# Optimization experiments

Hardware: AMD Instinct MI355X
Metric: run time of the kernel (lower is better)

## Reference

```python
import jax, jax.numpy as jnp
import numpy as np

N = 20000   # nodes
E = 320000  # edges (avg degree 16)
K = 3       # Chebyshev order


def _glorot(key, shape):
    fan_in, fan_out = shape[-2], shape[-1]
    lim = (6.0 / (fan_in + fan_out)) ** 0.5
    return jax.random.uniform(key, shape, minval=-lim, maxval=lim, dtype=jnp.float32)


def setup_inputs() -> dict:
    key = jax.random.key(0)
    ks = jax.random.split(key, 8)
    v = jax.random.normal(ks[0], (N, 86), dtype=jnp.float32)
    edges = jax.random.randint(ks[1], (2, E), 0, N, dtype=jnp.int32)
    W1 = _glorot(ks[2], (K, 86, 128));  b1 = jnp.zeros((128,), jnp.float32)
    W2 = _glorot(ks[3], (K, 128, 256)); b2 = jnp.zeros((256,), jnp.float32)
    W3 = _glorot(ks[4], (K, 256, 512)); b3 = jnp.zeros((512,), jnp.float32)
    return {"v": v, "edges": edges, "W1": W1, "b1": b1,
            "W2": W2, "b2": b2, "W3": W3, "b3": b3}


def _cheb_norm(edges, n):
    # PyG ChebConv with sym norm, lambda_max=2: L_hat = L - I = -D^-1/2 A D^-1/2
    # (diagonal entries from get_laplacian (+1) and add_self_loops (-1) cancel).
    # Self loops are removed before computing the Laplacian -> mask them out.
    row, col = edges[0], edges[1]
    w = (row != col).astype(jnp.float32)
    deg = jax.ops.segment_sum(w, row, num_segments=n)
    dinv = jnp.where(deg > 0, jax.lax.rsqrt(jnp.maximum(deg, 1e-12)), 0.0)
    norm_w = -dinv[row] * w * dinv[col]  # [E]
    return row, col, norm_w


def _cheb_conv(x, row, col, norm_w, W, b):
    # W: [K, in, out]
    def prop(z):  # L_hat @ z via edge gather + segment scatter-add
        return jax.ops.segment_sum(norm_w[:, None] * z[col], row, num_segments=x.shape[0])
    Tx0 = x
    out = Tx0 @ W[0]
    Tx1 = prop(Tx0)
    out = out + Tx1 @ W[1]
    Tx2 = 2.0 * prop(Tx1) - Tx0
    out = out + Tx2 @ W[2]
    return out + b


def reference(v, edges, W1, b1, W2, b2, W3, b3):
    row, col, norm_w = _cheb_norm(edges, v.shape[0])
    nk = jax.random.key(42)
    x1 = jax.nn.relu(_cheb_conv(v, row, col, norm_w, W1, b1))
    x1 = x1 * jax.random.normal(jax.random.fold_in(nk, 1), x1.shape, x1.dtype)
    x2 = jax.nn.relu(_cheb_conv(x1, row, col, norm_w, W2, b2))
    x2 = x2 * jax.random.normal(jax.random.fold_in(nk, 2), x2.shape, x2.dtype)
    x3 = jax.nn.relu(_cheb_conv(x2, row, col, norm_w, W3, b3))
    x3 = x3 * jax.random.normal(jax.random.fold_in(nk, 3), x3.shape, x3.dtype)
    return (x1, x2, x3)
```

## Files before the change

### kernel.cpp

```cpp
#include <hip/hip_runtime.h>
#include <stdint.h>
#include <math.h>

#define DEV static __device__ __forceinline__

typedef __attribute__((ext_vector_type(8))) short bf16x8;
typedef __attribute__((ext_vector_type(4))) float f32x4;
typedef __attribute__((ext_vector_type(8))) unsigned short u16x8;

DEV uint32_t rotl32(uint32_t v, int d) { return (v << d) | (v >> (32 - d)); }

DEV void threefry2x32(uint32_t k0, uint32_t k1, uint32_t& x0, uint32_t& x1) {
  const uint32_t k2 = k0 ^ k1 ^ 0x1BD11BDAu;
  x0 += k0; x1 += k1;
#define TFR(R) { x0 += x1; x1 = rotl32(x1, R) ^ x0; }
  TFR(13) TFR(15) TFR(26) TFR(6)
  x0 += k1; x1 += k2 + 1u;
  TFR(17) TFR(29) TFR(16) TFR(24)
  x0 += k2; x1 += k0 + 2u;
  TFR(13) TFR(15) TFR(26) TFR(6)
  x0 += k0; x1 += k1 + 3u;
  TFR(17) TFR(29) TFR(16) TFR(24)
  x0 += k1; x1 += k2 + 4u;
  TFR(13) TFR(15) TFR(26) TFR(6)
  x0 += k2; x1 += k0 + 5u;
#undef TFR
}

DEV float erfinv_f32(float x) {
  float w = -log1pf(-x * x);
  float p;
  if (w < 5.0f) {
    w -= 2.5f;
    p = 2.81022636e-08f;
    p = fmaf(p, w, 3.43273939e-07f);
    p = fmaf(p, w, -3.5233877e-06f);
    p = fmaf(p, w, -4.39150654e-06f);
    p = fmaf(p, w, 0.00021858087f);
    p = fmaf(p, w, -0.00125372503f);
    p = fmaf(p, w, -0.00417768164f);
    p = fmaf(p, w, 0.246640727f);
    p = fmaf(p, w, 1.50140941f);
  } else {
    w = sqrtf(w) - 3.0f;
    p = -0.000200214257f;
    p = fmaf(p, w, 0.000100950558f);
    p = fmaf(p, w, 0.00134934322f);
    p = fmaf(p, w, -0.00367342844f);
    p = fmaf(p, w, 0.00573950773f);
    p = fmaf(p, w, -0.0076224613f);
    p = fmaf(p, w, 0.00943887047f);
    p = fmaf(p, w, 1.00167406f);
    p = fmaf(p, w, 2.83297682f);
  }
  return p * x;
}

DEV float normal_from_bits(uint32_t bits) {
  float f = __uint_as_float((bits >> 9) | 0x3F800000u) - 1.0f;
  const float lo = -0.99999994f;
  float u = fmaf(f, 2.0f, lo);
  u = fmaxf(u, lo);
  return 1.41421356f * erfinv_f32(u);
}

DEV unsigned short f2bf(float f) {
  uint32_t u = __float_as_uint(f);
  uint32_t r = u + 0x7FFFu + ((u >> 16) & 1u);
  return (unsigned short)(r >> 16);
}

DEV float bf2f(uint32_t h) { return __uint_as_float(h << 16); }

DEV float4 noise4(uint32_t f0, uint32_t f1, uint32_t i4) {
  uint32_t base = i4 * 4u;
  float4 r;
  { uint32_t a = 0u, b = base + 0u; threefry2x32(f0, f1, a, b); r.x = normal_from_bits(a ^ b); }
  { uint32_t a = 0u, b = base + 1u; threefry2x32(f0, f1, a, b); r.y = normal_from_bits(a ^ b); }
  { uint32_t a = 0u, b = base + 2u; threefry2x32(f0, f1, a, b); r.z = normal_from_bits(a ^ b); }
  { uint32_t a = 0u, b = base + 3u; threefry2x32(f0, f1, a, b); r.w = normal_from_bits(a ^ b); }
  return r;
}

__global__ void count_kernel(const int* __restrict__ rows, const int* __restrict__ cols,
                             int* __restrict__ counts, int* __restrict__ degs, int E) {
  int e = blockIdx.x * blockDim.x + threadIdx.x;
  if (e < E) {
    int r = rows[e];
    atomicAdd(&counts[r], 1);
    if (r != cols[e]) atomicAdd(&degs[r], 1);
  }
}

#define SCAN_T 1024
__global__ __launch_bounds__(SCAN_T) void scan_kernel(const int* __restrict__ counts,
                                                      int* __restrict__ row_ptr,
                                                      int* __restrict__ cursor, int N) {
  __shared__ int sa[SCAN_T], sb[SCAN_T];
  const int t = threadIdx.x;
  const int CH = (N + SCAN_T - 1) / SCAN_T;
  int base = t * CH;
  int psum = 0;
  for (int k = 0; k < CH; ++k) {
    int idx = base + k;
    if (idx < N) psum += counts[idx];
  }
  sa[t] = psum;
  __syncthreads();
  int* src = sa; int* dst = sb;
  for (int off = 1; off < SCAN_T; off <<= 1) {
    int v = src[t];
    if (t >= off) v += src[t - off];
    dst[t] = v;
    __syncthreads();
    int* tmp = src; src = dst; dst = tmp;
  }
  int running = src[t] - psum;
  for (int k = 0; k < CH; ++k) {
    int idx = base + k;
    if (idx < N) {
      row_ptr[idx] = running;
      cursor[idx] = running;
      running += counts[idx];
    }
  }
  if (t == SCAN_T - 1) row_ptr[N] = running;
}

__global__ void fill_kernel(const int* __restrict__ rows, const int* __restrict__ cols,
                            const int* __restrict__ degs, int* __restrict__ cursor,
                            float2* __restrict__ ecv, int E) {
  int e = blockIdx.x * blockDim.x + threadIdx.x;
  if (e < E) {
    int r = rows[e], c = cols[e];
    int dr = degs[r], dc = degs[c];
    float w = (r != c && dr > 0 && dc > 0) ? -rsqrtf((float)dr) * rsqrtf((float)dc) : 0.0f;
    int pos = atomicAdd(&cursor[r], 1);
    ecv[pos] = make_float2(__int_as_float(c), w);
  }
}

__global__ void prep_kernel(const float* __restrict__ v,
                            const float* __restrict__ W1, const float* __restrict__ W2,
                            const float* __restrict__ W3,
                            unsigned short* __restrict__ vb, unsigned short* __restrict__ wt1,
                            unsigned short* __restrict__ wt2, unsigned short* __restrict__ wt3,
                            int N) {
  int i = blockIdx.x * 256 + threadIdx.x;
  int nv = N * 96;
  if (i < nv) {
    int r = i / 96, k = i % 96;
    vb[i] = (k < 86) ? f2bf(v[(size_t)r * 86 + k]) : (unsigned short)0;
    return;
  }
  i -= nv;
  if (i < 3 * 128 * 96) {
    int k = i % 96, o = (i / 96) % 128, p = i / (96 * 128);
    wt1[i] = (k < 86) ? f2bf(W1[((size_t)p * 86 + k) * 128 + o]) : (unsigned short)0;
    return;
  }
  i -= 3 * 128 * 96;
  if (i < 3 * 256 * 128) {
    int k = i % 128, o = (i / 128) % 256, p = i / (128 * 256);
    wt2[i] = f2bf(W2[((size_t)p * 128 + k) * 256 + o]);
    return;
  }
  i -= 3 * 256 * 128;
  if (i < 3 * 512 * 256) {
    int k = i % 256, o = (i / 256) % 512, p = i / (256 * 512);
    wt3[i] = f2bf(W3[((size_t)p * 256 + k) * 512 + o]);
  }
}

DEV void ld8(const unsigned short* __restrict__ base, size_t off, float* v) {
  uint4 u = *(const uint4*)(base + off);
  v[0] = bf2f(u.x & 0xffffu); v[1] = bf2f(u.x >> 16);
  v[2] = bf2f(u.y & 0xffffu); v[3] = bf2f(u.y >> 16);
  v[4] = bf2f(u.z & 0xffffu); v[5] = bf2f(u.z >> 16);
  v[6] = bf2f(u.w & 0xffffu); v[7] = bf2f(u.w >> 16);
}

template <int LPN, int NL, int SUB, int FOLD>
__global__ __launch_bounds__(256) void gather_prop(
    const int* __restrict__ row_ptr, const float2* __restrict__ ecv,
    const unsigned short* __restrict__ xsrc, int sstride,
    const float* __restrict__ xsub, int substride, int F,
    unsigned short* __restrict__ outb, int N, int Fpad,
    unsigned short* __restrict__ nbuf, int n4_begin, int n4_end) {
  const int wave = threadIdx.x >> 6, lane = threadIdx.x & 63;
  const int sub = lane / LPN;
  const int fl = (lane - sub * LPN) * 8;
  const int node = (blockIdx.x * 4 + wave) * NL + sub;
  if (sub < NL && node < N) {
    float acc[8] = {};
    const int s = row_ptr[node], e = row_ptr[node + 1];
    int j = s;
    for (; j + 8 <= e; j += 8) {
      float2 cw[8];
      float vv[8][8];
#pragma unroll
      for (int q = 0; q < 8; ++q) cw[q] = ecv[j + q];
#pragma unroll
      for (int q = 0; q < 8; ++q)
        ld8(xsrc, (size_t)__float_as_int(cw[q].x) * sstride + fl, vv[q]);
#pragma unroll
      for (int q = 0; q < 8; ++q)
#pragma unroll
        for (int z = 0; z < 8; ++z) acc[z] = fmaf(cw[q].y, vv[q][z], acc[z]);
    }
    for (; j + 2 <= e; j += 2) {
      float2 cw[2];
      float vv[2][8];
#pragma unroll
      for (int q = 0; q < 2; ++q) cw[q] = ecv[j + q];
#pragma unroll
      for (int q = 0; q < 2; ++q)
        ld8(xsrc, (size_t)__float_as_int(cw[q].x) * sstride + fl, vv[q]);
#pragma unroll
      for (int q = 0; q < 2; ++q)
#pragma unroll
        for (int z = 0; z < 8; ++z) acc[z] = fmaf(cw[q].y, vv[q][z], acc[z]);
    }
    for (; j < e; ++j) {
      float2 cw = ecv[j];
      float vv[8];
      ld8(xsrc, (size_t)__float_as_int(cw.x) * sstride + fl, vv);
#pragma unroll
      for (int z = 0; z < 8; ++z) acc[z] = fmaf(cw.y, vv[z], acc[z]);
    }
    if (SUB) {
      const float* sb = xsub + (size_t)node * substride;
      if (fl + 8 <= F) {
        float4 a = *(const float4*)(sb + fl);
        float4 b2 = *(const float4*)(sb + fl + 4);
        acc[0] = fmaf(2.0f, acc[0], -a.x);  acc[1] = fmaf(2.0f, acc[1], -a.y);
        acc[2] = fmaf(2.0f, acc[2], -a.z);  acc[3] = fmaf(2.0f, acc[3], -a.w);
        acc[4] = fmaf(2.0f, acc[4], -b2.x); acc[5] = fmaf(2.0f, acc[5], -b2.y);
        acc[6] = fmaf(2.0f, acc[6], -b2.z); acc[7] = fmaf(2.0f, acc[7], -b2.w);
      } else {
#pragma unroll
        for (int z = 0; z < 8; ++z) {
          int f = fl + z;
          float sv = (f < F) ? sb[f] : 0.0f;
          acc[z] = fmaf(2.0f, acc[z], -sv);
        }
      }
    }
    uint4 u;
    u.x = (uint32_t)f2bf(acc[0]) | ((uint32_t)f2bf(acc[1]) << 16);
    u.y = (uint32_t)f2bf(acc[2]) | ((uint32_t)f2bf(acc[3]) << 16);
    u.z = (uint32_t)f2bf(acc[4]) | ((uint32_t)f2bf(acc[5]) << 16);
    u.w = (uint32_t)f2bf(acc[6]) | ((uint32_t)f2bf(acc[7]) << 16);
    *(uint4*)&outb[(size_t)node * Fpad + fl] = u;
  }
  uint32_t f0k = 0u, f1k = (uint32_t)FOLD;
  threefry2x32(0u, 42u, f0k, f1k);
  const int gstride = gridDim.x * 256;
  for (int i4 = n4_begin + blockIdx.x * 256 + (int)threadIdx.x; i4 < n4_end; i4 += gstride) {
    float4 r = noise4(f0k, f1k, (uint32_t)i4);
    uint2 u;
    u.x = (uint32_t)f2bf(r.x) | ((uint32_t)f2bf(r.y) << 16);
    u.y = (uint32_t)f2bf(r.z) | ((uint32_t)f2bf(r.w) << 16);
    *(uint2*)&nbuf[(size_t)i4 * 4] = u;
  }
}

template <int BM, int FPAD, int KS, int OB>
__global__ __launch_bounds__(512, 4) void gemm3_db(
    const unsigned short* __restrict__ A0, const unsigned short* __restrict__ A1,
    const unsigned short* __restrict__ A2,
    const unsigned short* __restrict__ Wt, const float* __restrict__ bias,
    const unsigned short* __restrict__ noise,
    int M, int MT, int O, float* __restrict__ out, unsigned short* __restrict__ outb,
    int obstride) {
  constexpr int BN = 128;
  constexpr int NSP = FPAD / KS;
  constexpr int NSTEP = 3 * NSP;
  constexpr int CPR = KS / 8;
  constexpr int LST = KS + 8;
  constexpr int NA = BM * CPR;
  constexpr int NB = BN * CPR;
  constexpr int ACH = (NA + 511) / 512;
  constexpr int BCH = (NB + 511) / 512;
  constexpr int MFR = BM / 32;
  constexpr int KK = KS / 32;

  const int flat = blockIdx.x;
  const int xcd = flat & 7, idx = flat >> 3;
  const int mtile = xcd + 8 * (idx / OB);
  const int obl = idx - (idx / OB) * OB;
  if (mtile >= MT) return;
  const int bm = mtile * BM;
  const int bo = obl * BN;

  __shared__ unsigned short sA[2][BM * LST];
  __shared__ unsigned short sB[2][BN * LST];

  const int tid = threadIdx.x;
  const int lane = tid & 63;
  const int wave = tid >> 6;
  const int wm = wave >> 2, wo = wave & 3;
  const int l15 = lane & 15;
  const int kg = (lane >> 4) * 8;

  f32x4 acc[MFR][2] = {};
  const unsigned short* As[3] = {A0, A1, A2};

  u16x8 ra0[ACH], rb0[BCH], ra1[ACH], rb1[BCH];

  auto issue = [&](int s, u16x8 (&ra)[ACH], u16x8 (&rb)[BCH]) {
    int p = s / NSP, k0 = (s % NSP) * KS;
    const unsigned short* __restrict__ A = As[p];
    const unsigned short* __restrict__ B = Wt + (size_t)p * O * FPAD;
#pragma unroll
    for (int c = 0; c < ACH; ++c) {
      int idx2 = tid + c * 512;
      if (NA % 512 == 0 || idx2 < NA) {
        int row = idx2 / CPR, ch = (idx2 % CPR) * 8;
        int gm = bm + row; if (gm >= M) gm = M - 1;
        ra[c] = *(const u16x8*)(A + (size_t)gm * FPAD + k0 + ch);
      }
    }
#pragma unroll
    for (int c = 0; c < BCH; ++c) {
      int idx2 = tid + c * 512;
      if (NB % 512 == 0 || idx2 < NB) {
        int row = idx2 / CPR, ch = (idx2 % CPR) * 8;
        rb[c] = *(const u16x8*)(B + (size_t)(bo + row) * FPAD + k0 + ch);
      }
    }
  };

  auto lds_write = [&](int buf, u16x8 (&ra)[ACH], u16x8 (&rb)[BCH]) {
#pragma unroll
    for (int c = 0; c < ACH; ++c) {
      int idx2 = tid + c * 512;
      if (NA % 512 == 0 || idx2 < NA) {
        int row = idx2 / CPR, ch = (idx2 % CPR) * 8;
        *(u16x8*)&sA[buf][row * LST + ch] = ra[c];
      }
    }
#pragma unroll
    for (int c = 0; c < BCH; ++c) {
      int idx2 = tid + c * 512;
      if (NB % 512 == 0 || idx2 < NB) {
        int row = idx2 / CPR, ch = (idx2 % CPR) * 8;
        *(u16x8*)&sB[buf][row * LST + ch] = rb[c];
      }
    }
  };

  auto compute = [&](int buf) {
#pragma unroll
    for (int kk = 0; kk < KK; ++kk) {
      bf16x8 af[MFR], bfr[2];
#pragma unroll
      for (int mi = 0; mi < MFR; ++mi)
        af[mi] = *(const bf16x8*)&sA[buf][(wm * (BM / 2) + mi * 16 + l15) * LST + kk * 32 + kg];
#pragma unroll
      for (int ni = 0; ni < 2; ++ni)
        bfr[ni] = *(const bf16x8*)&sB[buf][(wo * 32 + ni * 16 + l15) * LST + kk * 32 + kg];
#pragma unroll
      for (int mi = 0; mi < MFR; ++mi)
#pragma unroll
        for (int ni = 0; ni < 2; ++ni)
          acc[mi][ni] = __builtin_amdgcn_mfma_f32_16x16x32_bf16(af[mi], bfr[ni], acc[mi][ni], 0, 0, 0);
    }
  };

  issue(0, ra0, rb0);
  issue(1, ra1, rb1);
  lds_write(0, ra0, rb0);
  __syncthreads();

#pragma unroll
  for (int s = 0; s < NSTEP; ++s) {
    if ((s & 1) == 0) {
      if (s + 2 < NSTEP) issue(s + 2, ra0, rb0);
      compute(s & 1);
      if (s + 1 < NSTEP) { lds_write((s + 1) & 1, ra1, rb1); __syncthreads(); }
    } else {
      if (s + 2 < NSTEP) issue(s + 2, ra1, rb1);
      compute(s & 1);
      if (s + 1 < NSTEP) { lds_write((s + 1) & 1, ra0, rb0); __syncthreads(); }
    }
  }

  const int r0 = (lane >> 4) * 4;
#pragma unroll
  for (int mi = 0; mi < MFR; ++mi) {
#pragma unroll
    for (int r = 0; r < 4; ++r) {
      int gm = bm + wm * (BM / 2) + mi * 16 + r0 + r;
      if (gm >= M) continue;
#pragma unroll
      for (int ni = 0; ni < 2; ++ni) {
        int go = bo + wo * 32 + ni * 16 + l15;
        float vv = acc[mi][ni][r] + bias[go];
        vv = vv > 0.0f ? vv : 0.0f;
        float res = vv * bf2f((uint32_t)noise[(size_t)gm * O + go]);
        out[(size_t)gm * O + go] = res;
        if (outb) outb[(size_t)gm * obstride + go] = f2bf(res);
      }
    }
  }
}

extern "C" void kernel_launch(void* const* d_in, const int* in_sizes, int n_in,
                              void* d_out, int out_size, void* d_ws, size_t ws_size,
                              hipStream_t stream) {
  const float* v    = (const float*)d_in[0];
  const int*  edges = (const int*)d_in[1];
  const float* W1 = (const float*)d_in[2];
  const float* b1 = (const float*)d_in[3];
  const float* W2 = (const float*)d_in[4];
  const float* b2 = (const float*)d_in[5];
  const float* W3 = (const float*)d_in[6];
  const float* b3 = (const float*)d_in[7];
  float* out = (float*)d_out;

  const int N = in_sizes[0] / 86;
  const int E = in_sizes[1] / 2;
  const int* rows = edges;
  const int* cols = edges + E;

  uintptr_t cur = (uintptr_t)d_ws;
  auto alloc = [&](size_t bytes) {
    cur = (cur + 15) & ~(uintptr_t)15;
    void* p = (void*)cur;
    cur += bytes;
    return p;
  };
  float2* ecv          = (float2*)alloc((size_t)E * 8);
  int* counts          = (int*)alloc((size_t)N * 4);
  int* degs            = (int*)alloc((size_t)N * 4);
  int* row_ptr         = (int*)alloc((size_t)(N + 1) * 4);
  int* cursor          = (int*)alloc((size_t)N * 4);
  unsigned short* tx1b = (unsigned short*)alloc((size_t)N * 256 * 2);
  unsigned short* tx2b = (unsigned short*)alloc((size_t)N * 256 * 2);
  unsigned short* vb   = (unsigned short*)alloc((size_t)N * 96 * 2);
  unsigned short* x1b  = (unsigned short*)alloc((size_t)N * 128 * 2);
  unsigned short* x2b  = (unsigned short*)alloc((size_t)N * 256 * 2);
  unsigned short* wt1  = (unsigned short*)alloc((size_t)3 * 128 * 96 * 2);
  unsigned short* wt2  = (unsigned short*)alloc((size_t)3 * 256 * 128 * 2);
  unsigned short* wt3  = (unsigned short*)alloc((size_t)3 * 512 * 256 * 2);
  unsigned short* nbuf = (unsigned short*)alloc((size_t)N * 512 * 2);

  float* x1 = out;
  float* x2 = x1 + (size_t)N * 128;
  float* x3 = x2 + (size_t)N * 256;

  hipMemsetAsync(counts, 0, (size_t)2 * N * sizeof(int), stream);
  count_kernel<<<(E + 255) / 256, 256, 0, stream>>>(rows, cols, counts, degs, E);
  scan_kernel<<<1, SCAN_T, 0, stream>>>(counts, row_ptr, cursor, N);
  fill_kernel<<<(E + 255) / 256, 256, 0, stream>>>(rows, cols, degs, cursor, ecv, E);
  {
    int total = N * 96 + 3 * 128 * 96 + 3 * 256 * 128 + 3 * 512 * 256;
    prep_kernel<<<(total + 255) / 256, 256, 0, stream>>>(v, W1, W2, W3, vb, wt1, wt2, wt3, N);
  }

  {
    int pb = (N + 15) / 16;
    int t4 = N * 128 / 4, h4 = t4 / 2;
    gather_prop<12, 4, 0, 1><<<pb, 256, 0, stream>>>(row_ptr, ecv, vb, 96, nullptr, 0, 86, tx1b, N, 96, nbuf, 0, h4);
    gather_prop<12, 4, 1, 1><<<pb, 256, 0, stream>>>(row_ptr, ecv, tx1b, 96, v, 86, 86, tx2b, N, 96, nbuf, h4, t4);
    int mt = (N + 63) / 64;
    int grid = 8 * ((mt + 7) / 8) * 1;
    gemm3_db<64, 96, 32, 1><<<grid, 512, 0, stream>>>(vb, tx1b, tx2b, wt1, b1, nbuf, N, mt, 128, x1, x1b, 128);
  }
  {
    int pb = (N + 15) / 16;
    int t4 = N * 256 / 4, h4 = t4 / 2;
    gather_prop<16, 4, 0, 2><<<pb, 256, 0, stream>>>(row_ptr, ecv, x1b, 128, nullptr, 0, 128, tx1b, N, 128, nbuf, 0, h4);
    gather_prop<16, 4, 1, 2><<<pb, 256, 0, stream>>>(row_ptr, ecv, tx1b, 128, x1, 128, 128, tx2b, N, 128, nbuf, h4, t4);
    int mt = (N + 127) / 128;
    int grid = 8 * ((mt + 7) / 8) * 2;
    gemm3_db<128, 128, 64, 2><<<grid, 512, 0, stream>>>(x1b, tx1b, tx2b, wt2, b2, nbuf, N, mt, 256, x2, x2b, 256);
  }
  {
    int pb = (N + 7) / 8;
    int t4 = N * 512 / 4, h4 = t4 / 2;
    gather_prop<32, 2, 0, 3><<<pb, 256, 0, stream>>>(row_ptr, ecv, x2b, 256, nullptr, 0, 256, tx1b, N, 256, nbuf, 0, h4);
    gather_prop<32, 2, 1, 3><<<pb, 256, 0, stream>>>(row_ptr, ecv, tx1b, 256, x2, 256, 256, tx2b, N, 256, nbuf, h4, t4);
    int mt = (N + 127) / 128;
    int grid = 8 * ((mt + 7) / 8) * 4;
    gemm3_db<128, 256, 64, 4><<<grid, 512, 0, stream>>>(x2b, tx1b, tx2b, wt3, b3, nbuf, N, mt, 512, x3, nullptr, 0);
  }
}
```

Baseline: 360.7 us.

## Fold Chebyshev T2 recurrence into weights and move noise generation into GEMM tails

Rewrites the Chebyshev combination algebraically: W0' = W0 - W2 and W2' = 2*W2 are precomputed in prep, so the second propagation becomes a plain L_hat application with no fp32 x read and subtract. This removes the SUB path and its extra fp32 loads from gather_prop. Noise generation also moves out of the gather kernels. Layer-1 noise is now produced in prep_kernel, and the next layer's noise is generated at the end of each GEMM kernel into separate buffers (nb1 aliases nb3). Precision changes slightly, since W0-W2 is rounded to bf16 together and Tx2 is no longer formed explicitly.

Result: slower. 416.4 us (+15.4%).

```diff
diff --git a/kernel.cpp b/kernel.cpp
--- a/kernel.cpp
+++ b/kernel.cpp
@@ -82,6 +82,19 @@
   return r;
 }
 
+DEV void noise_fill(unsigned short* __restrict__ nb, int total4, int fold,
+                    int gbase, int gstride) {
+  uint32_t f0k = 0u, f1k = (uint32_t)fold;
+  threefry2x32(0u, 42u, f0k, f1k);
+  for (int i4 = gbase; i4 < total4; i4 += gstride) {
+    float4 r = noise4(f0k, f1k, (uint32_t)i4);
+    uint2 u;
+    u.x = (uint32_t)f2bf(r.x) | ((uint32_t)f2bf(r.y) << 16);
+    u.y = (uint32_t)f2bf(r.z) | ((uint32_t)f2bf(r.w) << 16);
+    *(uint2*)&nb[(size_t)i4 * 4] = u;
+  }
+}
+
 __global__ void count_kernel(const int* __restrict__ rows, const int* __restrict__ cols,
                              int* __restrict__ counts, int* __restrict__ degs, int E) {
   int e = blockIdx.x * blockDim.x + threadIdx.x;
@@ -145,7 +158,9 @@
                             const float* __restrict__ W3,
                             unsigned short* __restrict__ vb, unsigned short* __restrict__ wt1,
                             unsigned short* __restrict__ wt2, unsigned short* __restrict__ wt3,
-                            int N) {
+                            unsigned short* __restrict__ nb1, int n1_total4, int N) {
+  noise_fill(nb1, n1_total4, 1, blockIdx.x * 256 + threadIdx.x, gridDim.x * 256);
+
   int i = blockIdx.x * 256 + threadIdx.x;
   int nv = N * 96;
   if (i < nv) {
@@ -156,19 +171,33 @@
   i -= nv;
   if (i < 3 * 128 * 96) {
     int k = i % 96, o = (i / 96) % 128, p = i / (96 * 128);
-    wt1[i] = (k < 86) ? f2bf(W1[((size_t)p * 86 + k) * 128 + o]) : (unsigned short)0;
+    float val = 0.0f;
+    if (k < 86) {
+      if (p == 0)      val = W1[((size_t)0 * 86 + k) * 128 + o] - W1[((size_t)2 * 86 + k) * 128 + o];
+      else if (p == 1) val = W1[((size_t)1 * 86 + k) * 128 + o];
+      else             val = 2.0f * W1[((size_t)2 * 86 + k) * 128 + o];
+    }
+    wt1[i] = (k < 86) ? f2bf(val) : (unsigned short)0;
     return;
   }
   i -= 3 * 128 * 96;
   if (i < 3 * 256 * 128) {
     int k = i % 128, o = (i / 128) % 256, p = i / (128 * 256);
-    wt2[i] = f2bf(W2[((size_t)p * 128 + k) * 256 + o]);
+    float val;
+    if (p == 0)      val = W2[((size_t)0 * 128 + k) * 256 + o] - W2[((size_t)2 * 128 + k) * 256 + o];
+    else if (p == 1) val = W2[((size_t)1 * 128 + k) * 256 + o];
+    else             val = 2.0f * W2[((size_t)2 * 128 + k) * 256 + o];
+    wt2[i] = f2bf(val);
     return;
   }
   i -= 3 * 256 * 128;
   if (i < 3 * 512 * 256) {
     int k = i % 256, o = (i / 256) % 512, p = i / (256 * 512);
-    wt3[i] = f2bf(W3[((size_t)p * 256 + k) * 512 + o]);
+    float val;
+    if (p == 0)      val = W3[((size_t)0 * 256 + k) * 512 + o] - W3[((size_t)2 * 256 + k) * 512 + o];
+    else if (p == 1) val = W3[((size_t)1 * 256 + k) * 512 + o];
+    else             val = 2.0f * W3[((size_t)2 * 256 + k) * 512 + o];
+    wt3[i] = f2bf(val);
   }
 }
 
@@ -180,89 +209,58 @@
   v[6] = bf2f(u.w & 0xffffu); v[7] = bf2f(u.w >> 16);
 }
 
-template <int LPN, int NL, int SUB, int FOLD>
+template <int LPN, int NL>
 __global__ __launch_bounds__(256) void gather_prop(
     const int* __restrict__ row_ptr, const float2* __restrict__ ecv,
     const unsigned short* __restrict__ xsrc, int sstride,
-    const float* __restrict__ xsub, int substride, int F,
-    unsigned short* __restrict__ outb, int N, int Fpad,
-    unsigned short* __restrict__ nbuf, int n4_begin, int n4_end) {
+    unsigned short* __restrict__ outb, int N, int Fpad) {
   const int wave = threadIdx.x >> 6, lane = threadIdx.x & 63;
   const int sub = lane / LPN;
   const int fl = (lane - sub * LPN) * 8;
   const int node = (blockIdx.x * 4 + wave) * NL + sub;
-  if (sub < NL && node < N) {
-    float acc[8] = {};
-    const int s = row_ptr[node], e = row_ptr[node + 1];
-    int j = s;
-    for (; j + 8 <= e; j += 8) {
-      float2 cw[8];
-      float vv[8][8];
-#pragma unroll
-      for (int q = 0; q < 8; ++q) cw[q] = ecv[j + q];
-#pragma unroll
-      for (int q = 0; q < 8; ++q)
-        ld8(xsrc, (size_t)__float_as_int(cw[q].x) * sstride + fl, vv[q]);
-#pragma unroll
-      for (int q = 0; q < 8; ++q)
-#pragma unroll
-        for (int z = 0; z < 8; ++z) acc[z] = fmaf(cw[q].y, vv[q][z], acc[z]);
-    }
-    for (; j + 2 <= e; j += 2) {
-      float2 cw[2];
-      float vv[2][8];
-#pragma unroll
-      for (int q = 0; q < 2; ++q) cw[q] = ecv[j + q];
-#pragma unroll
-      for (int q = 0; q < 2; ++q)
-        ld8(xsrc, (size_t)__float_as_int(cw[q].x) * sstride + fl, vv[q]);
-#pragma unroll
-      for (int q = 0; q < 2; ++q)
-#pragma unroll
-        for (int z = 0; z < 8; ++z) acc[z] = fmaf(cw[q].y, vv[q][z], acc[z]);
-    }
-    for (; j < e; ++j) {
-      float2 cw = ecv[j];
-      float vv[8];
-      ld8(xsrc, (size_t)__float_as_int(cw.x) * sstride + fl, vv);
-#pragma unroll
-      for (int z = 0; z < 8; ++z) acc[z] = fmaf(cw.y, vv[z], acc[z]);
-    }
-    if (SUB) {
-      const float* sb = xsub + (size_t)node * substride;
-      if (fl + 8 <= F) {
-        float4 a = *(const float4*)(sb + fl);
-        float4 b2 = *(const float4*)(sb + fl + 4);
-        acc[0] = fmaf(2.0f, acc[0], -a.x);  acc[1] = fmaf(2.0f, acc[1], -a.y);
-        acc[2] = fmaf(2.0f, acc[2], -a.z);  acc[3] = fmaf(2.0f, acc[3], -a.w);
-        acc[4] = fmaf(2.0f, acc[4], -b2.x); acc[5] = fmaf(2.0f, acc[5], -b2.y);
-        acc[6] = fmaf(2.0f, acc[6], -b2.z); acc[7] = fmaf(2.0f, acc[7], -b2.w);
-      } else {
-#pragma unroll
-        for (int z = 0; z < 8; ++z) {
-          int f = fl + z;
-          float sv = (f < F) ? sb[f] : 0.0f;
-          acc[z] = fmaf(2.0f, acc[z], -sv);
-        }
-      }
-    }
-    uint4 u;
-    u.x = (uint32_t)f2bf(acc[0]) | ((uint32_t)f2bf(acc[1]) << 16);
-    u.y = (uint32_t)f2bf(acc[2]) | ((uint32_t)f2bf(acc[3]) << 16);
-    u.z = (uint32_t)f2bf(acc[4]) | ((uint32_t)f2bf(acc[5]) << 16);
-    u.w = (uint32_t)f2bf(acc[6]) | ((uint32_t)f2bf(acc[7]) << 16);
-    *(uint4*)&outb[(size_t)node * Fpad + fl] = u;
-  }
-  uint32_t f0k = 0u, f1k = (uint32_t)FOLD;
-  threefry2x32(0u, 42u, f0k, f1k);
-  const int gstride = gridDim.x * 256;
-  for (int i4 = n4_begin + blockIdx.x * 256 + (int)threadIdx.x; i4 < n4_end; i4 += gstride) {
-    float4 r = noise4(f0k, f1k, (uint32_t)i4);
-    uint2 u;
-    u.x = (uint32_t)f2bf(r.x) | ((uint32_t)f2bf(r.y) << 16);
-    u.y = (uint32_t)f2bf(r.z) | ((uint32_t)f2bf(r.w) << 16);
-    *(uint2*)&nbuf[(size_t)i4 * 4] = u;
-  }
+  if (sub >= NL || node >= N) return;
+  float acc[8] = {};
+  const int s = row_ptr[node], e = row_ptr[node + 1];
+  int j = s;
+  for (; j + 8 <= e; j += 8) {
+    float2 cw[8];
+    float vv[8][8];
+#pragma unroll
+    for (int q = 0; q < 8; ++q) cw[q] = ecv[j + q];
+#pragma unroll
+    for (int q = 0; q < 8; ++q)
+      ld8(xsrc, (size_t)__float_as_int(cw[q].x) * sstride + fl, vv[q]);
+#pragma unroll
+    for (int q = 0; q < 8; ++q)
+#pragma unroll
+      for (int z = 0; z < 8; ++z) acc[z] = fmaf(cw[q].y, vv[q][z], acc[z]);
+  }
+  for (; j + 2 <= e; j += 2) {
+    float2 cw[2];
+    float vv[2][8];
+#pragma unroll
+    for (int q = 0; q < 2; ++q) cw[q] = ecv[j + q];
+#pragma unroll
+    for (int q = 0; q < 2; ++q)
+      ld8(xsrc, (size_t)__float_as_int(cw[q].x) * sstride + fl, vv[q]);
+#pragma unroll
+    for (int q = 0; q < 2; ++q)
+#pragma unroll
+      for (int z = 0; z < 8; ++z) acc[z] = fmaf(cw[q].y, vv[q][z], acc[z]);
+  }
+  for (; j < e; ++j) {
+    float2 cw = ecv[j];
+    float vv[8];
+    ld8(xsrc, (size_t)__float_as_int(cw.x) * sstride + fl, vv);
+#pragma unroll
+    for (int z = 0; z < 8; ++z) acc[z] = fmaf(cw.y, vv[z], acc[z]);
+  }
+  uint4 u;
+  u.x = (uint32_t)f2bf(acc[0]) | ((uint32_t)f2bf(acc[1]) << 16);
+  u.y = (uint32_t)f2bf(acc[2]) | ((uint32_t)f2bf(acc[3]) << 16);
+  u.z = (uint32_t)f2bf(acc[4]) | ((uint32_t)f2bf(acc[5]) << 16);
+  u.w = (uint32_t)f2bf(acc[6]) | ((uint32_t)f2bf(acc[7]) << 16);
+  *(uint4*)&outb[(size_t)node * Fpad + fl] = u;
 }
 
 template <int BM, int FPAD, int KS, int OB>
@@ -272,7 +270,7 @@
     const unsigned short* __restrict__ Wt, const float* __restrict__ bias,
     const unsigned short* __restrict__ noise,
     int M, int MT, int O, float* __restrict__ out, unsigned short* __restrict__ outb,
-    int obstride) {
+    int obstride, unsigned short* __restrict__ nnext, int ntotal4, int nfold) {
   constexpr int BN = 128;
   constexpr int NSP = FPAD / KS;
   constexpr int NSTEP = 3 * NSP;
@@ -289,121 +287,126 @@
   const int xcd = flat & 7, idx = flat >> 3;
   const int mtile = xcd + 8 * (idx / OB);
   const int obl = idx - (idx / OB) * OB;
-  if (mtile >= MT) return;
-  const int bm = mtile * BM;
-  const int bo = obl * BN;
 
   __shared__ unsigned short sA[2][BM * LST];
   __shared__ unsigned short sB[2][BN * LST];
 
   const int tid = threadIdx.x;
-  const int lane = tid & 63;
-  const int wave = tid >> 6;
-  const int wm = wave >> 2, wo = wave & 3;
-  const int l15 = lane & 15;
-  const int kg = (lane >> 4) * 8;
-
-  f32x4 acc[MFR][2] = {};
-  const unsigned short* As[3] = {A0, A1, A2};
-
-  u16x8 ra0[ACH], rb0[BCH], ra1[ACH], rb1[BCH];
-
-  auto issue = [&](int s, u16x8 (&ra)[ACH], u16x8 (&rb)[BCH]) {
-    int p = s / NSP, k0 = (s % NSP) * KS;
-    const unsigned short* __restrict__ A = As[p];
-    const unsigned short* __restrict__ B = Wt + (size_t)p * O * FPAD;
-#pragma unroll
-    for (int c = 0; c < ACH; ++c) {
-      int idx2 = tid + c * 512;
-      if (NA % 512 == 0 || idx2 < NA) {
-        int row = idx2 / CPR, ch = (idx2 % CPR) * 8;
-        int gm = bm + row; if (gm >= M) gm = M - 1;
-        ra[c] = *(const u16x8*)(A + (size_t)gm * FPAD + k0 + ch);
+
+  if (mtile < MT) {
+    const int bm = mtile * BM;
+    const int bo = obl * BN;
+    const int lane = tid & 63;
+    const int wave = tid >> 6;
+    const int wm = wave >> 2, wo = wave & 3;
+    const int l15 = lane & 15;
+    const int kg = (lane >> 4) * 8;
+
+    f32x4 acc[MFR][2] = {};
+    const unsigned short* As[3] = {A0, A1, A2};
+
+    u16x8 ra0[ACH], rb0[BCH], ra1[ACH], rb1[BCH];
+
+    auto issue = [&](int s, u16x8 (&ra)[ACH], u16x8 (&rb)[BCH]) {
+      int p = s / NSP, k0 = (s % NSP) * KS;
+      const unsigned short* __restrict__ A = As[p];
+      const unsigned short* __restrict__ B = Wt + (size_t)p * O * FPAD;
+#pragma unroll
+      for (int c = 0; c < ACH; ++c) {
+        int idx2 = tid + c * 512;
+        if (NA % 512 == 0 || idx2 < NA) {
+          int row = idx2 / CPR, ch = (idx2 % CPR) * 8;
+          int gm = bm + row; if (gm >= M) gm = M - 1;
+          ra[c] = *(const u16x8*)(A + (size_t)gm * FPAD + k0 + ch);
+        }
+      }
+#pragma unroll
+      for (int c = 0; c < BCH; ++c) {
+        int idx2 = tid + c * 512;
+        if (NB % 512 == 0 || idx2 < NB) {
+          int row = idx2 / CPR, ch = (idx2 % CPR) * 8;
+          rb[c] = *(const u16x8*)(B + (size_t)(bo + row) * FPAD + k0 + ch);
+        }
+      }
+    };
+
+    auto lds_write = [&](int buf, u16x8 (&ra)[ACH], u16x8 (&rb)[BCH]) {
+#pragma unroll
+      for (int c = 0; c < ACH; ++c) {
+        int idx2 = tid + c * 512;
+        if (NA % 512 == 0 || idx2 < NA) {
+          int row = idx2 / CPR, ch = (idx2 % CPR) * 8;
+          *(u16x8*)&sA[buf][row * LST + ch] = ra[c];
+        }
+      }
+#pragma unroll
+      for (int c = 0; c < BCH; ++c) {
+        int idx2 = tid + c * 512;
+        if (NB % 512 == 0 || idx2 < NB) {
+          int row = idx2 / CPR, ch = (idx2 % CPR) * 8;
+          *(u16x8*)&sB[buf][row * LST + ch] = rb[c];
+        }
+      }
+    };
+
+    auto compute = [&](int buf) {
+#pragma unroll
+      for (int kk = 0; kk < KK; ++kk) {
+        bf16x8 af[MFR], bfr[2];
+#pragma unroll
+        for (int mi = 0; mi < MFR; ++mi)
+          af[mi] = *(const bf16x8*)&sA[buf][(wm * (BM / 2) + mi * 16 + l15) * LST + kk * 32 + kg];
+#pragma unroll
+        for (int ni = 0; ni < 2; ++ni)
+          bfr[ni] = *(const bf16x8*)&sB[buf][(wo * 32 + ni * 16 + l15) * LST + kk * 32 + kg];
+#pragma unroll
+        for (int mi = 0; mi < MFR; ++mi)
+#pragma unroll
+          for (int ni = 0; ni < 2; ++ni)
+            acc[mi][ni] = __builtin_amdgcn_mfma_f32_16x16x32_bf16(af[mi], bfr[ni], acc[mi][ni], 0, 0, 0);
+      }
+    };
+
+    issue(0, ra0, rb0);
+    issue(1, ra1, rb1);
+    lds_write(0, ra0, rb0);
+    __syncthreads();
+
+#pragma unroll
+    for (int s = 0; s < NSTEP; ++s) {
+      if ((s & 1) == 0) {
+        if (s + 2 < NSTEP) issue(s + 2, ra0, rb0);
+        compute(s & 1);
+        if (s + 1 < NSTEP) { lds_write((s + 1) & 1, ra1, rb1); __syncthreads(); }
+      } else {
+        if (s + 2 < NSTEP) issue(s + 2, ra1, rb1);
+        compute(s & 1);
+        if (s + 1 < NSTEP) { lds_write((s + 1) & 1, ra0, rb0); __syncthreads(); }
       }
     }
-#pragma unroll
-    for (int c = 0; c < BCH; ++c) {
-      int idx2 = tid + c * 512;
-      if (NB % 512 == 0 || idx2 < NB) {
-        int row = idx2 / CPR, ch = (idx2 % CPR) * 8;
-        rb[c] = *(const u16x8*)(B + (size_t)(bo + row) * FPAD + k0 + ch);
+
+    const int r0 = (lane >> 4) * 4;
+#pragma unroll
+    for (int mi = 0; mi < MFR; ++mi) {
+#pragma unroll
+      for (int r = 0; r < 4; ++r) {
+        int gm = bm + wm * (BM / 2) + mi * 16 + r0 + r;
+        if (gm >= M) continue;
+#pragma unroll
+        for (int ni = 0; ni < 2; ++ni) {
+          int go = bo + wo * 32 + ni * 16 + l15;
+          float vv = acc[mi][ni][r] + bias[go];
+          vv = vv > 0.0f ? vv : 0.0f;
+          float res = vv * bf2f((uint32_t)noise[(size_t)gm * O + go]);
+          out[(size_t)gm * O + go] = res;
+          if (outb) outb[(size_t)gm * obstride + go] = f2bf(res);
+        }
       }
     }
-  };
-
-  auto lds_write = [&](int buf, u16x8 (&ra)[ACH], u16x8 (&rb)[BCH]) {
-#pragma unroll
-    for (int c = 0; c < ACH; ++c) {
-      int idx2 = tid + c * 512;
-      if (NA % 512 == 0 || idx2 < NA) {
-        int row = idx2 / CPR, ch = (idx2 % CPR) * 8;
-        *(u16x8*)&sA[buf][row * LST + ch] = ra[c];
-      }
-    }
-#pragma unroll
-    for (int c = 0; c < BCH; ++c) {
-      int idx2 = tid + c * 512;
-      if (NB % 512 == 0 || idx2 < NB) {
-        int row = idx2 / CPR, ch = (idx2 % CPR) * 8;
-        *(u16x8*)&sB[buf][row * LST + ch] = rb[c];
-      }
-    }
-  };
-
-  auto compute = [&](int buf) {
-#pragma unroll
-    for (int kk = 0; kk < KK; ++kk) {
-      bf16x8 af[MFR], bfr[2];
-#pragma unroll
-      for (int mi = 0; mi < MFR; ++mi)
-        af[mi] = *(const bf16x8*)&sA[buf][(wm * (BM / 2) + mi * 16 + l15) * LST + kk * 32 + kg];
-#pragma unroll
-      for (int ni = 0; ni < 2; ++ni)
-        bfr[ni] = *(const bf16x8*)&sB[buf][(wo * 32 + ni * 16 + l15) * LST + kk * 32 + kg];
-#pragma unroll
-      for (int mi = 0; mi < MFR; ++mi)
-#pragma unroll
-        for (int ni = 0; ni < 2; ++ni)
-          acc[mi][ni] = __builtin_amdgcn_mfma_f32_16x16x32_bf16(af[mi], bfr[ni], acc[mi][ni], 0, 0, 0);
-    }
-  };
-
-  issue(0, ra0, rb0);
-  issue(1, ra1, rb1);
-  lds_write(0, ra0, rb0);
-  __syncthreads();
-
-#pragma unroll
-  for (int s = 0; s < NSTEP; ++s) {
-    if ((s & 1) == 0) {
-      if (s + 2 < NSTEP) issue(s + 2, ra0, rb0);
-      compute(s & 1);
-      if (s + 1 < NSTEP) { lds_write((s + 1) & 1, ra1, rb1); __syncthreads(); }
-    } else {
-      if (s + 2 < NSTEP) issue(s + 2, ra1, rb1);
-      compute(s & 1);
-      if (s + 1 < NSTEP) { lds_write((s + 1) & 1, ra0, rb0); __syncthreads(); }
-    }
-  }
-
-  const int r0 = (lane >> 4) * 4;
-#pragma unroll
-  for (int mi = 0; mi < MFR; ++mi) {
-#pragma unroll
-    for (int r = 0; r < 4; ++r) {
-      int gm = bm + wm * (BM / 2) + mi * 16 + r0 + r;
-      if (gm >= M) continue;
-#pragma unroll
-      for (int ni = 0; ni < 2; ++ni) {
-        int go = bo + wo * 32 + ni * 16 + l15;
-        float vv = acc[mi][ni][r] + bias[go];
-        vv = vv > 0.0f ? vv : 0.0f;
-        float res = vv * bf2f((uint32_t)noise[(size_t)gm * O + go]);
-        out[(size_t)gm * O + go] = res;
-        if (outb) outb[(size_t)gm * obstride + go] = f2bf(res);
-      }
-    }
-  }
+  }
+
+  if (nnext)
+    noise_fill(nnext, ntotal4, nfold, blockIdx.x * 512 + tid, gridDim.x * 512);
 }
 
 extern "C" void kernel_launch(void* const* d_in, const int* in_sizes, int n_in,
@@ -444,7 +447,9 @@
   unsigned short* wt1  = (unsigned short*)alloc((size_t)3 * 128 * 96 * 2);
   unsigned short* wt2  = (unsigned short*)alloc((size_t)3 * 256 * 128 * 2);
   unsigned short* wt3  = (unsigned short*)alloc((size_t)3 * 512 * 256 * 2);
-  unsigned short* nbuf = (unsigned short*)alloc((size_t)N * 512 * 2);
+  unsigned short* nb2  = (unsigned short*)alloc((size_t)N * 256 * 2);
+  unsigned short* nb3  = (unsigned short*)alloc((size_t)N * 512 * 2);
+  unsigned short* nb1  = nb3;
 
   float* x1 = out;
   float* x2 = x1 + (size_t)N * 128;
@@ -456,34 +461,38 @@
   fill_kernel<<<(E + 255) / 256, 256, 0, stream>>>(rows, cols, degs, cursor, ecv, E);
   {
     int total = N * 96 + 3 * 128 * 96 + 3 * 256 * 128 + 3 * 512 * 256;
-    prep_kernel<<<(total + 255) / 256, 256, 0, stream>>>(v, W1, W2, W3, vb, wt1, wt2, wt3, N);
+    prep_kernel<<<(total + 255) / 256, 256, 0, stream>>>(v, W1, W2, W3, vb, wt1, wt2, wt3,
+                                                         nb1, N * 128 / 4, N);
   }
 
   {
     int pb = (N + 15) / 16;
-    int t4 = N * 128 / 4, h4 = t4 / 2;
-    gather_prop<12, 4, 0, 1><<<pb, 256, 0, stream>>>(row_ptr, ecv, vb, 96, nullptr, 0, 86, tx1b, N, 96, nbuf, 0, h4);
-    gather_prop<12, 4, 1, 1><<<pb, 256, 0, stream>>>(row_ptr, ecv, tx1b, 96, v, 86, 86, tx2b, N, 96, nbuf, h4, t4);
+    gather_prop<12, 4><<<pb, 256, 0, stream>>>(row_ptr, ecv, vb, 96, tx1b, N, 96);
+    gather_prop<12, 4><<<pb, 256, 0, stream>>>(row_ptr, ecv, tx1b, 96, tx2b, N, 96);
     int mt = (N + 63) / 64;
     int grid = 8 * ((mt + 7) / 8) * 1;
-    gemm3_db<64, 96, 32, 1><<<grid, 512, 0, stream>>>(vb, tx1b, tx2b, wt1, b1, nbuf, N, mt, 128, x1, x1b, 128);
+    gemm3_db<64, 96, 32, 1><<<grid, 512, 0, stream>>>(vb, tx1b, tx2b, wt1, b1, nb1,
+                                                      N, mt, 128, x1, x1b, 128,
+                                                      nb2, N * 256 / 4, 2);
   }
   {
     int pb = (N + 15) / 16;
-    int t4 = N * 256 / 4, h4 = t4 / 2;
-    gather_prop<16, 4, 0, 2><<<pb, 256, 0, stream>>>(row_ptr, ecv, x1b, 128, nullptr, 0, 128, tx1b, N, 128, nbuf, 0, h4);
-    gather_prop<16, 4, 1, 2><<<pb, 256, 0, stream>>>(row_ptr, ecv, tx1b, 128, x1, 128, 128, tx2b, N, 128, nbuf, h4, t4);
+    gather_prop<16, 4><<<pb, 256, 0, stream>>>(row_ptr, ecv, x1b, 128, tx1b, N, 128);
+    gather_prop<16, 4><<<pb, 256, 0, stream>>>(row_ptr, ecv, tx1b, 128, tx2b, N, 128);
     int mt = (N + 127) / 128;
     int grid = 8 * ((mt + 7) / 8) * 2;
-    gemm3_db<128, 128, 64, 2><<<grid, 512, 0, stream>>>(x1b, tx1b, tx2b, wt2, b2, nbuf, N, mt, 256, x2, x2b, 256);
+    gemm3_db<128, 128, 64, 2><<<grid, 512, 0, stream>>>(x1b, tx1b, tx2b, wt2, b2, nb2,
+                                                        N, mt, 256, x2, x2b, 256,
+                                                        nb3, N * 512 / 4, 3);
   }
   {
     int pb = (N + 7) / 8;
-    int t4 = N * 512 / 4, h4 = t4 / 2;
-    gather_prop<32, 2, 0, 3><<<pb, 256, 0, stream>>>(row_ptr, ecv, x2b, 256, nullptr, 0, 256, tx1b, N, 256, nbuf, 0, h4);
-    gather_prop<32, 2, 1, 3><<<pb, 256, 0, stream>>>(row_ptr, ecv, tx1b, 256, x2, 256, 256, tx2b, N, 256, nbuf, h4, t4);
+    gather_prop<32, 2><<<pb, 256, 0, stream>>>(row_ptr, ecv, x2b, 256, tx1b, N, 256);
+    gather_prop<32, 2><<<pb, 256, 0, stream>>>(row_ptr, ecv, tx1b, 256, tx2b, N, 256);
     int mt = (N + 127) / 128;
     int grid = 8 * ((mt + 7) / 8) * 4;
-    gemm3_db<128, 256, 64, 4><<<grid, 512, 0, stream>>>(x2b, tx1b, tx2b, wt3, b3, nbuf, N, mt, 512, x3, nullptr, 0);
-  }
-}
+    gemm3_db<128, 256, 64, 4><<<grid, 512, 0, stream>>>(x2b, tx1b, tx2b, wt3, b3, nb3,
+                                                        N, mt, 512, x3, nullptr, 0,
+                                                        nullptr, 0, 0);
+  }
+}
```
